# Performance work log

Hardware: AMD Instinct MI355X
Metric: run time of the kernel (lower is better)

The kernel has to match this reference:

```python
import jax, jax.numpy as jnp
import numpy as np

FACTOR = 2  # self.factor; anchor='edge', interpolation='linear', bound='dft', extrapolate=False


def _resize_axis_linear_dft(x, axis, osz):
    """Linear resize of one axis with periodic ('dft') boundary, anchor='edge'.

    Out-of-FOV samples (|coord| beyond [-0.5, isz-0.5]) are zeroed
    (extrapolate=False). With edge anchor this mask is always all-True,
    but we keep it for faithfulness.
    """
    isz = x.shape[axis]
    # edge anchor: output voxel centers map to input coords
    c = (jnp.arange(osz, dtype=x.dtype) + 0.5) * (isz / osz) - 0.5
    i0 = jnp.floor(c).astype(jnp.int32)
    w1 = c - i0.astype(x.dtype)          # fractional part
    i0w = jnp.mod(i0, isz)               # dft = circular wrap
    i1w = jnp.mod(i0 + 1, isz)
    x0 = jnp.take(x, i0w, axis=axis)
    x1 = jnp.take(x, i1w, axis=axis)
    # broadcast weights along `axis`
    bshape = [1] * x.ndim
    bshape[axis] = osz
    w1b = w1.reshape(bshape)
    inb = ((c >= -0.5) & (c <= isz - 0.5)).astype(x.dtype).reshape(bshape)
    return (x0 * (1.0 - w1b) + x1 * w1b) * inb


def _resize_flow(flow):
    # flow: (batch, ndim, *inshape)
    ishape = flow.shape[2:]
    oshape = tuple(int(s * FACTOR) for s in ishape)
    out = flow
    for d, osz in enumerate(oshape):
        out = _resize_axis_linear_dft(out, axis=2 + d, osz=osz)
    # anchor 'e': rescale displacement magnitude per channel by osz/isz
    scales = jnp.array([o / i for o, i in zip(oshape, ishape)], dtype=flow.dtype)
    scales = scales.reshape((1, len(ishape)) + (1,) * len(ishape))
    return out * scales


def setup_inputs() -> dict:
    key = jax.random.key(0)
    flow = jax.random.normal(key, (2, 3, 96, 96, 96), dtype=jnp.float32)
    return {"flow": flow}


def reference(flow):
    return _resize_flow(flow)
```

## Files before the change

kernel.cpp:

```cpp
#include <hip/hip_runtime.h>


#define ISZ  96
#define OSZ  192
#define NX4  48
#define ZSTR (ISZ * ISZ)

typedef float vf4 __attribute__((ext_vector_type(4)));

struct Q4 { float a, b, c, d; };

__global__ __launch_bounds__(256)
void resize_flow_kernel(const float* __restrict__ in, float* __restrict__ out) {
    unsigned bid = blockIdx.x;
    unsigned wid = (bid & 7u) * (gridDim.x >> 3) + (bid >> 3);
    unsigned t   = wid * 256u + threadIdx.x;

    int x4 = (int)(t % NX4);
    unsigned r = t / NX4;
    int ky = (int)(r % ISZ); r /= ISZ;
    int kz = (int)(r % ISZ);
    int bc = (int)(r / ISZ);

    int kzm = (kz == 0)       ? ISZ - 1 : kz - 1;
    int kzp = (kz == ISZ - 1) ? 0       : kz + 1;
    int kym = (ky == 0)       ? ISZ - 1 : ky - 1;
    int kyp = (ky == ISZ - 1) ? 0       : ky + 1;

    int xm = 2 * x4;
    int xa = (x4 == 0)       ? ISZ - 1 : xm - 1;
    int xd = (x4 == NX4 - 1) ? 0       : xm + 2;

    const float* base = in + (size_t)bc * (ISZ * ZSTR);

    auto ld = [&](const float* row) -> Q4 {
        float2 m = *reinterpret_cast<const float2*>(row + xm);
        Q4 q; q.a = row[xa]; q.b = m.x; q.c = m.y; q.d = row[xd];
        return q;
    };

    auto yblend = [&](const float* pz, Q4& A, Q4& B) {
        Q4 rm = ld(pz + kym * ISZ);
        Q4 r0 = ld(pz + ky  * ISZ);
        Q4 rp = ld(pz + kyp * ISZ);
        A.a = fmaf(0.25f, rm.a, 0.75f * r0.a);
        A.b = fmaf(0.25f, rm.b, 0.75f * r0.b);
        A.c = fmaf(0.25f, rm.c, 0.75f * r0.c);
        A.d = fmaf(0.25f, rm.d, 0.75f * r0.d);
        B.a = fmaf(0.25f, rp.a, 0.75f * r0.a);
        B.b = fmaf(0.25f, rp.b, 0.75f * r0.b);
        B.c = fmaf(0.25f, rp.c, 0.75f * r0.c);
        B.d = fmaf(0.25f, rp.d, 0.75f * r0.d);
    };

    Q4 Am, Bm, A0, B0, Ap, Bp;
    yblend(base + (size_t)kzm * ZSTR, Am, Bm);
    yblend(base + (size_t)kz  * ZSTR, A0, B0);
    yblend(base + (size_t)kzp * ZSTR, Ap, Bp);

    auto zblend = [](float wl, const Q4& L, float wh, const Q4& H) -> Q4 {
        Q4 q;
        q.a = fmaf(wl, L.a, wh * H.a);
        q.b = fmaf(wl, L.b, wh * H.b);
        q.c = fmaf(wl, L.c, wh * H.c);
        q.d = fmaf(wl, L.d, wh * H.d);
        return q;
    };
    Q4 q00 = zblend(0.5f, Am, 1.5f, A0);
    Q4 q01 = zblend(0.5f, Bm, 1.5f, B0);
    Q4 q10 = zblend(1.5f, A0, 0.5f, Ap);
    Q4 q11 = zblend(1.5f, B0, 0.5f, Bp);

    auto xstore = [&](const Q4& q, int oz, int oy) {
        vf4 o;
        o.x = fmaf(0.25f, q.a, 0.75f * q.b);
        o.y = fmaf(0.25f, q.c, 0.75f * q.b);
        o.z = fmaf(0.25f, q.b, 0.75f * q.c);
        o.w = fmaf(0.25f, q.d, 0.75f * q.c);
        float* p = out + (((size_t)bc * OSZ + oz) * OSZ + oy) * OSZ + 4 * x4;
        __builtin_nontemporal_store(o, reinterpret_cast<vf4*>(p));
    };
    xstore(q00, 2 * kz,     2 * ky);
    xstore(q01, 2 * kz,     2 * ky + 1);
    xstore(q10, 2 * kz + 1, 2 * ky);
    xstore(q11, 2 * kz + 1, 2 * ky + 1);
}

extern "C" void kernel_launch(void* const* d_in, const int* in_sizes, int n_in,
                              void* d_out, int out_size, void* d_ws, size_t ws_size,
                              hipStream_t stream) {
    const float* in = (const float*)d_in[0];
    float* out = (float*)d_out;

    int total = 6 * ISZ * ISZ * NX4;
    int block = 256;
    int grid  = total / block;

    resize_flow_kernel<<<grid, block, 0, stream>>>(in, out);
}
```

Measured before the change: 42.10 us.

## Register-block 2x2 input rows per thread to reuse neighbor loads in resize

Measured after the change: 36.60 us. -13.1%, faster.

```diff
diff --git a/kernel.cpp b/kernel.cpp
--- a/kernel.cpp
+++ b/kernel.cpp
@@ -4,11 +4,30 @@
 #define ISZ  96
 #define OSZ  192
 #define NX4  48
+#define NT   48
 #define ZSTR (ISZ * ISZ)
 
 typedef float vf4 __attribute__((ext_vector_type(4)));
 
 struct Q4 { float a, b, c, d; };
+
+__device__ __forceinline__ Q4 q_wsum(float wl, const Q4& L, float wh, const Q4& H) {
+    Q4 q;
+    q.a = fmaf(wl, L.a, wh * H.a);
+    q.b = fmaf(wl, L.b, wh * H.b);
+    q.c = fmaf(wl, L.c, wh * H.c);
+    q.d = fmaf(wl, L.d, wh * H.d);
+    return q;
+}
+__device__ __forceinline__ Q4 q_scale(float w, const Q4& Y) {
+    Q4 q; q.a = w * Y.a; q.b = w * Y.b; q.c = w * Y.c; q.d = w * Y.d; return q;
+}
+__device__ __forceinline__ void q_acc(Q4& O, float w, const Q4& Y) {
+    O.a = fmaf(w, Y.a, O.a);
+    O.b = fmaf(w, Y.b, O.b);
+    O.c = fmaf(w, Y.c, O.c);
+    O.d = fmaf(w, Y.d, O.d);
+}
 
 __global__ __launch_bounds__(256)
 void resize_flow_kernel(const float* __restrict__ in, float* __restrict__ out) {
@@ -18,18 +37,23 @@
 
     int x4 = (int)(t % NX4);
     unsigned r = t / NX4;
-    int ky = (int)(r % ISZ); r /= ISZ;
-    int kz = (int)(r % ISZ);
-    int bc = (int)(r / ISZ);
-
-    int kzm = (kz == 0)       ? ISZ - 1 : kz - 1;
-    int kzp = (kz == ISZ - 1) ? 0       : kz + 1;
-    int kym = (ky == 0)       ? ISZ - 1 : ky - 1;
-    int kyp = (ky == ISZ - 1) ? 0       : ky + 1;
+    int ty = (int)(r % NT); r /= NT;
+    int tz = (int)(r % NT);
+    int bc = (int)(r / NT);
 
     int xm = 2 * x4;
     int xa = (x4 == 0)       ? ISZ - 1 : xm - 1;
     int xd = (x4 == NX4 - 1) ? 0       : xm + 2;
+
+    int ky  = 2 * ty;
+    int ry0 = (ky == 0) ? ISZ - 1 : ky - 1;
+    int ry1 = ky, ry2 = ky + 1;
+    int ry3 = (ky + 2 == ISZ) ? 0 : ky + 2;
+
+    int kz  = 2 * tz;
+    int pz0 = (kz == 0) ? ISZ - 1 : kz - 1;
+    int pz1 = kz, pz2 = kz + 1;
+    int pz3 = (kz + 2 == ISZ) ? 0 : kz + 2;
 
     const float* base = in + (size_t)bc * (ISZ * ZSTR);
 
@@ -39,51 +63,58 @@
         return q;
     };
 
-    auto yblend = [&](const float* pz, Q4& A, Q4& B) {
-        Q4 rm = ld(pz + kym * ISZ);
-        Q4 r0 = ld(pz + ky  * ISZ);
-        Q4 rp = ld(pz + kyp * ISZ);
-        A.a = fmaf(0.25f, rm.a, 0.75f * r0.a);
-        A.b = fmaf(0.25f, rm.b, 0.75f * r0.b);
-        A.c = fmaf(0.25f, rm.c, 0.75f * r0.c);
-        A.d = fmaf(0.25f, rm.d, 0.75f * r0.d);
-        B.a = fmaf(0.25f, rp.a, 0.75f * r0.a);
-        B.b = fmaf(0.25f, rp.b, 0.75f * r0.b);
-        B.c = fmaf(0.25f, rp.c, 0.75f * r0.c);
-        B.d = fmaf(0.25f, rp.d, 0.75f * r0.d);
+    auto yblend = [&](int p, Q4& Y0, Q4& Y1, Q4& Y2, Q4& Y3) {
+        const float* pp = base + (size_t)p * ZSTR;
+        Q4 R0 = ld(pp + ry0 * ISZ);
+        Q4 R1 = ld(pp + ry1 * ISZ);
+        Q4 R2 = ld(pp + ry2 * ISZ);
+        Q4 R3 = ld(pp + ry3 * ISZ);
+        Y0 = q_wsum(0.25f, R0, 0.75f, R1);
+        Y1 = q_wsum(0.75f, R1, 0.25f, R2);
+        Y2 = q_wsum(0.25f, R1, 0.75f, R2);
+        Y3 = q_wsum(0.75f, R2, 0.25f, R3);
     };
 
-    Q4 Am, Bm, A0, B0, Ap, Bp;
-    yblend(base + (size_t)kzm * ZSTR, Am, Bm);
-    yblend(base + (size_t)kz  * ZSTR, A0, B0);
-    yblend(base + (size_t)kzp * ZSTR, Ap, Bp);
-
-    auto zblend = [](float wl, const Q4& L, float wh, const Q4& H) -> Q4 {
-        Q4 q;
-        q.a = fmaf(wl, L.a, wh * H.a);
-        q.b = fmaf(wl, L.b, wh * H.b);
-        q.c = fmaf(wl, L.c, wh * H.c);
-        q.d = fmaf(wl, L.d, wh * H.d);
-        return q;
-    };
-    Q4 q00 = zblend(0.5f, Am, 1.5f, A0);
-    Q4 q01 = zblend(0.5f, Bm, 1.5f, B0);
-    Q4 q10 = zblend(1.5f, A0, 0.5f, Ap);
-    Q4 q11 = zblend(1.5f, B0, 0.5f, Bp);
-
-    auto xstore = [&](const Q4& q, int oz, int oy) {
+    int oyb = 4 * ty, ozb = 4 * tz;
+    auto xstore = [&](const Q4& q, int dz, int dy) {
         vf4 o;
         o.x = fmaf(0.25f, q.a, 0.75f * q.b);
-        o.y = fmaf(0.25f, q.c, 0.75f * q.b);
+        o.y = fmaf(0.75f, q.b, 0.25f * q.c);
         o.z = fmaf(0.25f, q.b, 0.75f * q.c);
-        o.w = fmaf(0.25f, q.d, 0.75f * q.c);
-        float* p = out + (((size_t)bc * OSZ + oz) * OSZ + oy) * OSZ + 4 * x4;
+        o.w = fmaf(0.75f, q.c, 0.25f * q.d);
+        float* p = out + (((size_t)bc * OSZ + (ozb + dz)) * OSZ + (oyb + dy)) * OSZ + 4 * x4;
         __builtin_nontemporal_store(o, reinterpret_cast<vf4*>(p));
     };
-    xstore(q00, 2 * kz,     2 * ky);
-    xstore(q01, 2 * kz,     2 * ky + 1);
-    xstore(q10, 2 * kz + 1, 2 * ky);
-    xstore(q11, 2 * kz + 1, 2 * ky + 1);
+
+    Q4 Y0, Y1, Y2, Y3;
+
+    yblend(pz0, Y0, Y1, Y2, Y3);
+    Q4 A0 = q_scale(0.5f, Y0), A1 = q_scale(0.5f, Y1),
+       A2 = q_scale(0.5f, Y2), A3 = q_scale(0.5f, Y3);
+
+    yblend(pz1, Y0, Y1, Y2, Y3);
+    q_acc(A0, 1.5f, Y0); q_acc(A1, 1.5f, Y1);
+    q_acc(A2, 1.5f, Y2); q_acc(A3, 1.5f, Y3);
+    xstore(A0, 0, 0); xstore(A1, 0, 1); xstore(A2, 0, 2); xstore(A3, 0, 3);
+    Q4 B0 = q_scale(1.5f, Y0), B1 = q_scale(1.5f, Y1),
+       B2 = q_scale(1.5f, Y2), B3 = q_scale(1.5f, Y3);
+    Q4 C0 = q_scale(0.5f, Y0), C1 = q_scale(0.5f, Y1),
+       C2 = q_scale(0.5f, Y2), C3 = q_scale(0.5f, Y3);
+
+    yblend(pz2, Y0, Y1, Y2, Y3);
+    q_acc(B0, 0.5f, Y0); q_acc(B1, 0.5f, Y1);
+    q_acc(B2, 0.5f, Y2); q_acc(B3, 0.5f, Y3);
+    xstore(B0, 1, 0); xstore(B1, 1, 1); xstore(B2, 1, 2); xstore(B3, 1, 3);
+    q_acc(C0, 1.5f, Y0); q_acc(C1, 1.5f, Y1);
+    q_acc(C2, 1.5f, Y2); q_acc(C3, 1.5f, Y3);
+    xstore(C0, 2, 0); xstore(C1, 2, 1); xstore(C2, 2, 2); xstore(C3, 2, 3);
+    Q4 D0 = q_scale(1.5f, Y0), D1 = q_scale(1.5f, Y1),
+       D2 = q_scale(1.5f, Y2), D3 = q_scale(1.5f, Y3);
+
+    yblend(pz3, Y0, Y1, Y2, Y3);
+    q_acc(D0, 0.5f, Y0); q_acc(D1, 0.5f, Y1);
+    q_acc(D2, 0.5f, Y2); q_acc(D3, 0.5f, Y3);
+    xstore(D0, 3, 0); xstore(D1, 3, 1); xstore(D2, 3, 2); xstore(D3, 3, 3);
 }
 
 extern "C" void kernel_launch(void* const* d_in, const int* in_sizes, int n_in,
@@ -92,7 +123,7 @@
     const float* in = (const float*)d_in[0];
     float* out = (float*)d_out;
 
-    int total = 6 * ISZ * ISZ * NX4;
+    int total = 6 * NT * NT * NX4;
     int block = 256;
     int grid  = total / block;
 
```
